# Kernel optimization log

Measured on AMD Instinct MI355X. Metric: run time of the kernel, lower is better.

The kernel has to match this reference:

```python
import jax, jax.numpy as jnp
from jax import lax
import numpy as np

DN = ('NCDHW', 'OIDHW', 'NCDHW')
ACTIVE_THRESH = 1


def setup_inputs() -> dict:
    key = jax.random.key(0)
    ks = jax.random.split(key, 10)
    B, D = 4, 64
    chans = [3, 64, 128, 256, 512]
    inp = {
        'x': jax.random.normal(ks[0], (B, 3, D, D, D), jnp.float32),
        'mask': jax.random.randint(ks[1], (B, D, D, D), 0, 20, jnp.int32),
    }
    for i in range(4):
        cin, cout = chans[i], chans[i + 1]
        fan_in = cin * 27
        scale = 1.0 / np.sqrt(fan_in)
        inp[f'w{i+1}'] = jax.random.normal(ks[2 + 2 * i], (cout, cin, 3, 3, 3), jnp.float32) * scale
        inp[f'b{i+1}'] = jax.random.normal(ks[3 + 2 * i], (cout,), jnp.float32) * scale
    return inp


def _sparse_block(x, m, w, b, stride):
    # SparseConv3d(k=3, pad=1) + SparseReLU: output active where 3^3 footprint hits an active input;
    # bias + relu applied only at active sites, inactive sites stay exactly 0 (spconv .dense() semantics).
    s = (stride,) * 3
    pad = [(1, 1)] * 3
    y = lax.conv_general_dilated(x, w, s, pad, dimension_numbers=DN)
    ones = jnp.ones((1, 1, 3, 3, 3), x.dtype)
    m_out = lax.conv_general_dilated(m[:, None].astype(x.dtype), ones, s, pad, dimension_numbers=DN) > 0
    y = jnp.where(m_out, jax.nn.relu(y + b[None, :, None, None, None]), jnp.zeros((), x.dtype))
    return y, m_out[:, 0]


def reference(x, mask, w1, b1, w2, b2, w3, b3, w4, b4):
    m = mask < ACTIVE_THRESH                       # [B,D,H,W] active voxels
    h = x * m[:, None].astype(x.dtype)             # zero inactive input features
    h, m = _sparse_block(h, m, w1, b1, 1)          # [B,64,64,64,64]
    h, m = _sparse_block(h, m, w2, b2, 2)          # [B,128,32,32,32]
    h, m = _sparse_block(h, m, w3, b3, 2)          # [B,256,16,16,16]
    h, m = _sparse_block(h, m, w4, b4, 2)          # [B,512,8,8,8]
    pooled = jnp.max(h, axis=(2, 3, 4))            # dense() + amax over D,H,W -> [B,512]
    return jax.nn.leaky_relu(pooled, negative_slope=0.2)
```

## Files before the change

### kernel.cpp

```cpp
#include <hip/hip_runtime.h>

typedef _Float16 f16;
typedef _Float16 half4 __attribute__((ext_vector_type(4)));
typedef _Float16 half8 __attribute__((ext_vector_type(8)));
typedef float f32x4 __attribute__((ext_vector_type(4)));

#define BATCH 4

__device__ __forceinline__ void gload16(const void* g, void* l) {
  __builtin_amdgcn_global_load_lds((const __attribute__((address_space(1))) unsigned int*)g,
                                   (__attribute__((address_space(3))) unsigned int*)l, 16, 0, 0);
}

__global__ __launch_bounds__(256) void zero_k(unsigned int* __restrict__ z) {
  z[threadIdx.x] = 0u;
}

__global__ __launch_bounds__(256) void wprep_k(const float* __restrict__ w,
                                               f16* __restrict__ w27, int COUT, int CIN) {
  int idx = blockIdx.x * 256 + threadIdx.x;
  int total = COUT * CIN * 27;
  if (idx >= total) return;
  int k = idx % 27;
  int t = idx / 27;
  int ci = t % CIN;
  int co = t / CIN;
  w27[((size_t)k * COUT + co) * CIN + ci] = (f16)w[idx];
}

__global__ __launch_bounds__(256) void wprep1_k(const float* __restrict__ w,
                                                f16* __restrict__ wf) {
  int idx = blockIdx.x * 256 + threadIdx.x;
  if (idx >= 64 * 128) return;
  int q = idx & 127, co = idx >> 7;
  int k = q >> 2, ci = q & 3;
  float v = (ci < 3 && k < 27) ? w[(co * 3 + ci) * 27 + k] : 0.f;
  wf[idx] = (f16)v;
}

__global__ __launch_bounds__(256) void xmask_k(const float* __restrict__ x,
                                               const int* __restrict__ mask,
                                               f16* __restrict__ xc) {
  const int D3 = 262144;
  int v = blockIdx.x * 256 + threadIdx.x;
  int b = blockIdx.y;
  bool act = mask[(size_t)b * D3 + v] < 1;
  const float* xb = x + (size_t)b * 3 * D3 + v;
  half4 o;
  o[0] = act ? (f16)xb[0] : (f16)0.f;
  o[1] = act ? (f16)xb[D3] : (f16)0.f;
  o[2] = act ? (f16)xb[2 * D3] : (f16)0.f;
  o[3] = (f16)0.f;
  *reinterpret_cast<half4*>(xc + ((size_t)b * D3 + v) * 4) = o;
}

__global__ __launch_bounds__(256) void dil_w_k(const int* __restrict__ mask,
                                               unsigned char* __restrict__ aw) {
  const int D3 = 262144;
  int t = blockIdx.x * 256 + threadIdx.x;
  int b = t >> 16;
  int v = (t & 65535) * 4;
  int w0 = v & 63;
  const int* mb = mask + (size_t)b * D3;
  int a[6];
  a[0] = (w0 > 0) ? (mb[v - 1] < 1) : 0;
  #pragma unroll
  for (int i = 0; i < 4; i++) a[i + 1] = mb[v + i] < 1;
  a[5] = (w0 < 60) ? (mb[v + 4] < 1) : 0;
  unsigned int o = 0;
  #pragma unroll
  for (int i = 0; i < 4; i++)
    o |= ((unsigned)(a[i] | a[i + 1] | a[i + 2])) << (8 * i);
  *reinterpret_cast<unsigned int*>(aw + (size_t)b * D3 + v) = o;
}

template<int STRIDE, int DIMSHIFT>
__global__ __launch_bounds__(256) void dil_hd_k(const unsigned char* __restrict__ ai,
                                                unsigned char* __restrict__ ao) {
  const int D3 = 262144;
  int t = blockIdx.x * 256 + threadIdx.x;
  int b = t >> 16;
  int v = (t & 65535) * 4;
  int c = (v >> DIMSHIFT) & 63;
  const unsigned char* ib = ai + (size_t)b * D3;
  unsigned int m = *reinterpret_cast<const unsigned int*>(ib + v);
  if (c > 0)  m |= *reinterpret_cast<const unsigned int*>(ib + v - STRIDE);
  if (c < 63) m |= *reinterpret_cast<const unsigned int*>(ib + v + STRIDE);
  *reinterpret_cast<unsigned int*>(ao + (size_t)b * D3 + v) = m;
}

template<int DIN, int DOUT>
__global__ __launch_bounds__(256) void dilate_s2_k(const unsigned char* __restrict__ mi,
                                                   unsigned char* __restrict__ mo) {
  const int Do3 = DOUT * DOUT * DOUT;
  int v = blockIdx.x * 256 + threadIdx.x;
  if (v >= Do3) return;
  int b = blockIdx.y;
  int ow = v % DOUT, t = v / DOUT, oh = t % DOUT, od = t / DOUT;
  const unsigned char* ib = mi + (size_t)b * DIN * DIN * DIN;
  int act = 0;
  for (int kd = 0; kd < 3; kd++) { int id = od * 2 - 1 + kd; if ((unsigned)id >= (unsigned)DIN) continue;
    for (int kh = 0; kh < 3; kh++) { int ih = oh * 2 - 1 + kh; if ((unsigned)ih >= (unsigned)DIN) continue;
      for (int kw = 0; kw < 3; kw++) { int iw = ow * 2 - 1 + kw; if ((unsigned)iw >= (unsigned)DIN) continue;
        act |= ib[((size_t)id * DIN + ih) * DIN + iw];
      } } }
  mo[(size_t)b * Do3 + v] = (unsigned char)(act ? 1 : 0);
}

template<int BM>
__global__ __launch_bounds__(256) void conv1_mfma_k(const f16* __restrict__ xc,
                                                    const f16* __restrict__ w1f,
                                                    const float* __restrict__ bias,
                                                    const unsigned char* __restrict__ mo,
                                                    f16* __restrict__ out) {
  const int D = 64, D3 = D * D * D, COUT = 64;
  constexpr int K = 128, LD = K + 8;
  constexpr int WM = 2, WN = 2;
  constexpr int MF = BM / (16 * WM), NF = 64 / (16 * WN);
  __shared__ __align__(16) f16 As[BM][LD];
  __shared__ __align__(16) f16 Bs[64][LD];

  const int tid = threadIdx.x, lane = tid & 63, wave = tid >> 6;
  const int wm = wave >> 1, wn = wave & 1;
  const int v0 = blockIdx.x * BM;
  const int b = blockIdx.y;
  const f16* xb = xc + (size_t)b * D3 * 4;

  for (int c = tid; c < 64 * (K / 8); c += 256) {
    int row = c >> 4, cc = c & 15;
    *reinterpret_cast<half8*>(&Bs[row][cc * 8]) =
        *reinterpret_cast<const half8*>(w1f + row * K + cc * 8);
  }
  {
    const int row = tid & (BM - 1);
    const int v = v0 + row;
    const int ow = v & 63, oh = (v >> 6) & 63, od = v >> 12;
    for (int e = tid; e < 32 * BM; e += 256) {
      int kslot = e / BM;
      half4 val = {};
      if (kslot < 27) {
        int kd = kslot / 9, r2 = kslot - kd * 9, kh = r2 / 3, kw = r2 - kh * 3;
        int id = od - 1 + kd, ih = oh - 1 + kh, iw = ow - 1 + kw;
        if ((unsigned)id < (unsigned)D && (unsigned)ih < (unsigned)D && (unsigned)iw < (unsigned)D)
          val = *reinterpret_cast<const half4*>(xb + (size_t)((id * D + ih) * D + iw) * 4);
      }
      *reinterpret_cast<half4*>(&As[row][kslot * 4]) = val;
    }
  }
  __syncthreads();

  f32x4 acc[MF][NF] = {};
  const int chanoff = (lane >> 4) << 3;
  const int arow = wm * MF * 16 + (lane & 15);
  const int brow = wn * NF * 16 + (lane & 15);
  #pragma unroll
  for (int q0 = 0; q0 < K; q0 += 32) {
    half8 a[MF], bb[NF];
    #pragma unroll
    for (int mf = 0; mf < MF; mf++)
      a[mf] = *reinterpret_cast<const half8*>(&As[arow + mf * 16][q0 + chanoff]);
    #pragma unroll
    for (int nf = 0; nf < NF; nf++)
      bb[nf] = *reinterpret_cast<const half8*>(&Bs[brow + nf * 16][q0 + chanoff]);
    #pragma unroll
    for (int mf = 0; mf < MF; mf++)
      #pragma unroll
      for (int nf = 0; nf < NF; nf++)
        acc[mf][nf] = __builtin_amdgcn_mfma_f32_16x16x32_f16(a[mf], bb[nf], acc[mf][nf], 0, 0, 0);
  }

  const unsigned char* mb = mo + (size_t)b * D3;
  f16* ob = out + (size_t)b * D3 * COUT;
  float bv[NF];
  #pragma unroll
  for (int nf = 0; nf < NF; nf++) bv[nf] = bias[wn * NF * 16 + nf * 16 + (lane & 15)];
  #pragma unroll
  for (int mf = 0; mf < MF; mf++) {
    #pragma unroll
    for (int r = 0; r < 4; r++) {
      int v = v0 + wm * MF * 16 + mf * 16 + ((lane >> 4) << 2) + r;
      bool act = mb[v] != 0;
      #pragma unroll
      for (int nf = 0; nf < NF; nf++) {
        int co = wn * NF * 16 + nf * 16 + (lane & 15);
        float val = acc[mf][nf][r] + bv[nf];
        val = act ? (val > 0.f ? val : 0.f) : 0.f;
        ob[(size_t)v * COUT + co] = (f16)val;
      }
    }
  }
}

template<int CIN, int COUT, int DIN, int DOUT, int BM, int BN, int WM, int WN, int SWZ>
__global__ __launch_bounds__(WM * WN * 64) void conv_mfma2_k(const f16* __restrict__ in,
                                                             const f16* __restrict__ w27,
                                                             const float* __restrict__ bias,
                                                             const unsigned char* __restrict__ mo,
                                                             const f16* __restrict__ zpage,
                                                             f16* __restrict__ out) {
  constexpr int NW = WM * WN;
  constexpr int MF = BM / (16 * WM), NF = BN / (16 * WN);
  constexpr int ROWB = CIN * 2;
  constexpr int CHUNKS = ROWB / 16;
  constexpr int RPI = 64 / CHUNKS;
  constexpr int A_IW = BM / RPI / NW;
  constexpr int B_IW = BN / RPI / NW;
  constexpr int D3o = DOUT * DOUT * DOUT;
  constexpr int LOGD = (DOUT == 32) ? 5 : ((DOUT == 16) ? 4 : 3);

  __shared__ __align__(16) char As[2][BM * ROWB];
  __shared__ __align__(16) char Bs[2][BN * ROWB];

  const int tid = threadIdx.x, lane = tid & 63, wave = tid >> 6;
  const int wm = wave / WN, wn = wave % WN;
  int bx = blockIdx.x;
  if (SWZ) {
    int cpx = gridDim.x >> 3;
    bx = (bx & 7) * cpx + (bx >> 3);
  }
  const int v0 = bx * BM, co0 = blockIdx.y * BN, b = blockIdx.z;
  const char* ib = (const char*)(in + (size_t)b * DIN * DIN * DIN * CIN);

  const int lrow = lane / CHUNKS;
  const int lchunk = lane % CHUNKS;
  int a_od[A_IW], a_oh[A_IW], a_ow[A_IW], a_cb[A_IW];
  #pragma unroll
  for (int i = 0; i < A_IW; i++) {
    int r = (wave * A_IW + i) * RPI + lrow;
    int v = v0 + r;
    a_ow[i] = v & (DOUT - 1);
    a_oh[i] = (v >> LOGD) & (DOUT - 1);
    a_od[i] = v >> (2 * LOGD);
    a_cb[i] = (lchunk ^ (r & 7)) * 16;
  }
  size_t b_ob[B_IW];
  #pragma unroll
  for (int i = 0; i < B_IW; i++) {
    int r = (wave * B_IW + i) * RPI + lrow;
    int g = lchunk ^ (r & 7);
    b_ob[i] = ((size_t)(co0 + r) * CIN + g * 8) * 2;
  }

  auto stage = [&](int buf, int k) {
    int kd = k / 9, r2 = k - kd * 9, kh = r2 / 3, kw = r2 - kh * 3;
    #pragma unroll
    for (int i = 0; i < A_IW; i++) {
      int id = 2 * a_od[i] - 1 + kd, ih = 2 * a_oh[i] - 1 + kh, iw = 2 * a_ow[i] - 1 + kw;
      bool inb = (unsigned)id < (unsigned)DIN && (unsigned)ih < (unsigned)DIN &&
                 (unsigned)iw < (unsigned)DIN;
      const char* src = inb
          ? ib + ((size_t)(id * DIN + ih) * DIN + iw) * ROWB + a_cb[i]
          : (const char*)zpage;
      gload16(src, &As[buf][(wave * A_IW + i) * 1024]);
    }
    const char* wk = (const char*)w27 + (size_t)k * COUT * CIN * 2;
    #pragma unroll
    for (int i = 0; i < B_IW; i++)
      gload16(wk + b_ob[i], &Bs[buf][(wave * B_IW + i) * 1024]);
  };

  f32x4 acc[MF][NF] = {};
  const int ll = lane & 15, lh = lane >> 4;
  const int ra0 = wm * MF * 16 + ll;
  const int rb0 = wn * NF * 16 + ll;
  const int rswa = ra0 & 7;
  const int rswb = rb0 & 7;

  stage(0, 0);
  __syncthreads();
  int cur = 0;
  for (int k = 0; k < 27; k++) {
    if (k < 26) stage(cur ^ 1, k + 1);
    #pragma unroll
    for (int ci0 = 0; ci0 < CIN; ci0 += 32) {
      const int q = (ci0 >> 3) + lh;
      half8 a[MF], bb[NF];
      #pragma unroll
      for (int mf = 0; mf < MF; mf++)
        a[mf] = *reinterpret_cast<const half8*>(
            &As[cur][(ra0 + mf * 16) * ROWB + ((q ^ rswa) * 16)]);
      #pragma unroll
      for (int nf = 0; nf < NF; nf++)
        bb[nf] = *reinterpret_cast<const half8*>(
            &Bs[cur][(rb0 + nf * 16) * ROWB + ((q ^ rswb) * 16)]);
      #pragma unroll
      for (int mf = 0; mf < MF; mf++)
        #pragma unroll
        for (int nf = 0; nf < NF; nf++)
          acc[mf][nf] = __builtin_amdgcn_mfma_f32_16x16x32_f16(a[mf], bb[nf], acc[mf][nf], 0, 0, 0);
    }
    __syncthreads();
    cur ^= 1;
  }

  const unsigned char* mb = mo + (size_t)b * D3o;
  f16* ob = out + (size_t)b * D3o * COUT;
  float bv[NF];
  #pragma unroll
  for (int nf = 0; nf < NF; nf++) bv[nf] = bias[co0 + wn * NF * 16 + nf * 16 + ll];
  #pragma unroll
  for (int mf = 0; mf < MF; mf++) {
    #pragma unroll
    for (int r = 0; r < 4; r++) {
      int v = v0 + wm * MF * 16 + mf * 16 + (lh << 2) + r;
      bool act = mb[v] != 0;
      #pragma unroll
      for (int nf = 0; nf < NF; nf++) {
        int co = co0 + wn * NF * 16 + nf * 16 + ll;
        float val = acc[mf][nf][r] + bv[nf];
        val = act ? (val > 0.f ? val : 0.f) : 0.f;
        ob[(size_t)v * COUT + co] = (f16)val;
      }
    }
  }
}

__global__ __launch_bounds__(256) void pool_k(const f16* __restrict__ h4,
                                              float* __restrict__ outp) {
  __shared__ float red[4][64];
  int b = blockIdx.y;
  int cl = threadIdx.x & 63;
  int co = blockIdx.x * 64 + cl;
  int vg = threadIdx.x >> 6;
  const f16* p = h4 + (size_t)b * 512 * 512;
  float m = 0.f;
  for (int v = vg * 128; v < vg * 128 + 128; v++) m = fmaxf(m, (float)p[(size_t)v * 512 + co]);
  red[vg][cl] = m;
  __syncthreads();
  if (threadIdx.x < 64) {
    m = fmaxf(fmaxf(red[0][threadIdx.x], red[1][threadIdx.x]),
              fmaxf(red[2][threadIdx.x], red[3][threadIdx.x]));
    float r = (m >= 0.f) ? m : 0.2f * m;
    outp[b * 512 + blockIdx.x * 64 + threadIdx.x] = r;
  }
}

extern "C" void kernel_launch(void* const* d_in, const int* in_sizes, int n_in,
                              void* d_out, int out_size, void* d_ws, size_t ws_size,
                              hipStream_t stream) {
  const float* x    = (const float*)d_in[0];
  const int*   mask = (const int*)d_in[1];
  const float* w1 = (const float*)d_in[2];
  const float* b1 = (const float*)d_in[3];
  const float* w2 = (const float*)d_in[4];
  const float* b2 = (const float*)d_in[5];
  const float* w3 = (const float*)d_in[6];
  const float* b3 = (const float*)d_in[7];
  const float* w4 = (const float*)d_in[8];
  const float* b4 = (const float*)d_in[9];
  float* outp = (float*)d_out;

  char* ws = (char*)d_ws;
  size_t off = 0;
  auto alloc = [&](size_t bytes) -> char* {
    char* p = ws + off;
    off = (off + bytes + 255) & ~(size_t)255;
    return p;
  };
  f16* wf1 = (f16*)alloc((size_t)64 * 128 * 2);
  f16* wf2 = (f16*)alloc((size_t)27 * 128 * 64 * 2);
  f16* wf3 = (f16*)alloc((size_t)27 * 256 * 128 * 2);
  f16* wf4 = (f16*)alloc((size_t)27 * 512 * 256 * 2);
  f16* zpg = (f16*)alloc(1024);
  f16* xc  = (f16*)alloc((size_t)BATCH * 262144 * 4 * 2);
  unsigned char* aw = (unsigned char*)alloc((size_t)BATCH * 262144);
  unsigned char* ah = (unsigned char*)alloc((size_t)BATCH * 262144);
  unsigned char* m1 = (unsigned char*)alloc((size_t)BATCH * 262144);
  unsigned char* m2 = (unsigned char*)alloc((size_t)BATCH * 32768);
  unsigned char* m3 = (unsigned char*)alloc((size_t)BATCH * 4096);
  unsigned char* m4 = (unsigned char*)alloc((size_t)BATCH * 512);
  f16* h1 = (f16*)alloc((size_t)BATCH * 262144 * 64 * 2);
  f16* h2 = (f16*)alloc((size_t)BATCH * 32768 * 128 * 2);
  f16* h3 = (f16*)alloc((size_t)BATCH * 4096 * 256 * 2);
  f16* h4 = (f16*)alloc((size_t)BATCH * 512 * 512 * 2);
  if (off > ws_size) return;

  zero_k<<<dim3(1), 256, 0, stream>>>((unsigned int*)zpg);
  wprep1_k<<<dim3((64 * 128 + 255) / 256), 256, 0, stream>>>(w1, wf1);
  wprep_k<<<dim3((128 * 64 * 27 + 255) / 256), 256, 0, stream>>>(w2, wf2, 128, 64);
  wprep_k<<<dim3((256 * 128 * 27 + 255) / 256), 256, 0, stream>>>(w3, wf3, 256, 128);
  wprep_k<<<dim3((512 * 256 * 27 + 255) / 256), 256, 0, stream>>>(w4, wf4, 512, 256);
  xmask_k<<<dim3(1024, BATCH), 256, 0, stream>>>(x, mask, xc);

  dil_w_k<<<dim3(BATCH * 65536 / 256), 256, 0, stream>>>(mask, aw);
  dil_hd_k<64, 6><<<dim3(BATCH * 65536 / 256), 256, 0, stream>>>(aw, ah);
  dil_hd_k<4096, 12><<<dim3(BATCH * 65536 / 256), 256, 0, stream>>>(ah, m1);
  dilate_s2_k<64, 32><<<dim3(128, BATCH), 256, 0, stream>>>(m1, m2);
  dilate_s2_k<32, 16><<<dim3(16, BATCH), 256, 0, stream>>>(m2, m3);
  dilate_s2_k<16, 8><<<dim3(2, BATCH), 256, 0, stream>>>(m3, m4);

  conv1_mfma_k<128><<<dim3(262144 / 128, BATCH), 256, 0, stream>>>(xc, wf1, b1, m1, h1);
  conv_mfma2_k<64, 128, 64, 32, 128, 128, 2, 2, 1>
      <<<dim3(256, 1, BATCH), 256, 0, stream>>>(h1, wf2, b2, m2, zpg, h2);
  conv_mfma2_k<128, 256, 32, 16, 64, 64, 2, 2, 0>
      <<<dim3(64, 4, BATCH), 256, 0, stream>>>(h2, wf3, b3, m3, zpg, h3);
  conv_mfma2_k<256, 512, 16, 8, 64, 64, 2, 2, 0>
      <<<dim3(8, 8, BATCH), 256, 0, stream>>>(h3, wf4, b4, m4, zpg, h4);

  pool_k<<<dim3(8, BATCH), 256, 0, stream>>>(h4, outp);
}
```

Baseline: 351.9 us.

## Store activations in zero-padded volumes to remove gather bounds checks

Activations and the masked input are written into volumes padded by one voxel on every side. Small new kernels zero the border voxels. The conv gather loops now add a constant per-tap offset to precomputed source pointers, so the per-load bounds checks, the zero-page fallback and the coordinate math are gone. In exchange the buffers grow slightly, several extra border-zeroing launches are added, and the padded input buffer reuses the layer-3 activation buffer's storage.

```diff
diff --git a/kernel.cpp b/kernel.cpp
--- a/kernel.cpp
+++ b/kernel.cpp
@@ -12,8 +12,18 @@
                                    (__attribute__((address_space(3))) unsigned int*)l, 16, 0, 0);
 }
 
-__global__ __launch_bounds__(256) void zero_k(unsigned int* __restrict__ z) {
-  z[threadIdx.x] = 0u;
+template<int DP, int ROWB>
+__global__ __launch_bounds__(256) void zborder_k(char* __restrict__ buf) {
+  int v = blockIdx.x * 256 + threadIdx.x;
+  int b = blockIdx.y;
+  if (v >= DP * DP * DP) return;
+  int w = v % DP; int t = v / DP; int h = t % DP; int d = t / DP;
+  bool border = (w == 0) | (w == DP - 1) | (h == 0) | (h == DP - 1) | (d == 0) | (d == DP - 1);
+  if (!border) return;
+  char* p = buf + ((size_t)b * DP * DP * DP + v) * ROWB;
+  #pragma unroll
+  for (int i = 0; i < ROWB; i += 8)
+    *reinterpret_cast<unsigned long long*>(p + i) = 0ull;
 }
 
 __global__ __launch_bounds__(256) void wprep_k(const float* __restrict__ w,
@@ -40,8 +50,8 @@
 
 __global__ __launch_bounds__(256) void xmask_k(const float* __restrict__ x,
                                                const int* __restrict__ mask,
-                                               f16* __restrict__ xc) {
-  const int D3 = 262144;
+                                               f16* __restrict__ xcp) {
+  const int D3 = 262144, PD = 66, PD3 = PD * PD * PD;
   int v = blockIdx.x * 256 + threadIdx.x;
   int b = blockIdx.y;
   bool act = mask[(size_t)b * D3 + v] < 1;
@@ -51,7 +61,9 @@
   o[1] = act ? (f16)xb[D3] : (f16)0.f;
   o[2] = act ? (f16)xb[2 * D3] : (f16)0.f;
   o[3] = (f16)0.f;
-  *reinterpret_cast<half4*>(xc + ((size_t)b * D3 + v) * 4) = o;
+  int ow = v & 63, oh = (v >> 6) & 63, od = v >> 12;
+  size_t pv = ((size_t)(od + 1) * PD + oh + 1) * PD + ow + 1;
+  *reinterpret_cast<half4*>(xcp + ((size_t)b * PD3 + pv) * 4) = o;
 }
 
 __global__ __launch_bounds__(256) void dil_w_k(const int* __restrict__ mask,
@@ -108,12 +120,12 @@
 }
 
 template<int BM>
-__global__ __launch_bounds__(256) void conv1_mfma_k(const f16* __restrict__ xc,
+__global__ __launch_bounds__(256) void conv1_mfma_k(const f16* __restrict__ xcp,
                                                     const f16* __restrict__ w1f,
                                                     const float* __restrict__ bias,
                                                     const unsigned char* __restrict__ mo,
-                                                    f16* __restrict__ out) {
-  const int D = 64, D3 = D * D * D, COUT = 64;
+                                                    f16* __restrict__ out ) {
+  const int D3 = 262144, COUT = 64, PD = 66, PD3 = PD * PD * PD;
   constexpr int K = 128, LD = K + 8;
   constexpr int WM = 2, WN = 2;
   constexpr int MF = BM / (16 * WM), NF = 64 / (16 * WN);
@@ -124,7 +136,7 @@
   const int wm = wave >> 1, wn = wave & 1;
   const int v0 = blockIdx.x * BM;
   const int b = blockIdx.y;
-  const f16* xb = xc + (size_t)b * D3 * 4;
+  const f16* xb = xcp + (size_t)b * PD3 * 4;
 
   for (int c = tid; c < 64 * (K / 8); c += 256) {
     int row = c >> 4, cc = c & 15;
@@ -135,14 +147,13 @@
     const int row = tid & (BM - 1);
     const int v = v0 + row;
     const int ow = v & 63, oh = (v >> 6) & 63, od = v >> 12;
+    const int base = (od * PD + oh) * PD + ow;
     for (int e = tid; e < 32 * BM; e += 256) {
       int kslot = e / BM;
       half4 val = {};
       if (kslot < 27) {
         int kd = kslot / 9, r2 = kslot - kd * 9, kh = r2 / 3, kw = r2 - kh * 3;
-        int id = od - 1 + kd, ih = oh - 1 + kh, iw = ow - 1 + kw;
-        if ((unsigned)id < (unsigned)D && (unsigned)ih < (unsigned)D && (unsigned)iw < (unsigned)D)
-          val = *reinterpret_cast<const half4*>(xb + (size_t)((id * D + ih) * D + iw) * 4);
+        val = *reinterpret_cast<const half4*>(xb + (size_t)(base + (kd * PD + kh) * PD + kw) * 4);
       }
       *reinterpret_cast<half4*>(&As[row][kslot * 4]) = val;
     }
@@ -170,34 +181,37 @@
   }
 
   const unsigned char* mb = mo + (size_t)b * D3;
-  f16* ob = out + (size_t)b * D3 * COUT;
+  f16* ob = out + (size_t)b * PD3 * COUT;
+  const int ll = lane & 15, lh = lane >> 4;
   float bv[NF];
   #pragma unroll
-  for (int nf = 0; nf < NF; nf++) bv[nf] = bias[wn * NF * 16 + nf * 16 + (lane & 15)];
+  for (int nf = 0; nf < NF; nf++) bv[nf] = bias[wn * NF * 16 + nf * 16 + ll];
   #pragma unroll
   for (int mf = 0; mf < MF; mf++) {
     #pragma unroll
     for (int r = 0; r < 4; r++) {
-      int v = v0 + wm * MF * 16 + mf * 16 + ((lane >> 4) << 2) + r;
+      int v = v0 + wm * MF * 16 + mf * 16 + (lh << 2) + r;
       bool act = mb[v] != 0;
+      int ow = v & 63, oh = (v >> 6) & 63, od = v >> 12;
+      size_t pv = ((size_t)(od + 1) * PD + oh + 1) * PD + ow + 1;
       #pragma unroll
       for (int nf = 0; nf < NF; nf++) {
-        int co = wn * NF * 16 + nf * 16 + (lane & 15);
+        int co = wn * NF * 16 + nf * 16 + ll;
         float val = acc[mf][nf][r] + bv[nf];
         val = act ? (val > 0.f ? val : 0.f) : 0.f;
-        ob[(size_t)v * COUT + co] = (f16)val;
+        ob[pv * COUT + co] = (f16)val;
       }
     }
   }
 }
 
-template<int CIN, int COUT, int DIN, int DOUT, int BM, int BN, int WM, int WN, int SWZ>
+template<int CIN, int COUT, int DIN, int DOUT, int BM, int BN, int WM, int WN, int SWZ, int OP>
 __global__ __launch_bounds__(WM * WN * 64) void conv_mfma2_k(const f16* __restrict__ in,
                                                              const f16* __restrict__ w27,
                                                              const float* __restrict__ bias,
                                                              const unsigned char* __restrict__ mo,
-                                                             const f16* __restrict__ zpage,
                                                              f16* __restrict__ out) {
+  constexpr int PD = DIN + 2, PDo = DOUT + 2;
   constexpr int NW = WM * WN;
   constexpr int MF = BM / (16 * WM), NF = BN / (16 * WN);
   constexpr int ROWB = CIN * 2;
@@ -219,44 +233,37 @@
     bx = (bx & 7) * cpx + (bx >> 3);
   }
   const int v0 = bx * BM, co0 = blockIdx.y * BN, b = blockIdx.z;
-  const char* ib = (const char*)(in + (size_t)b * DIN * DIN * DIN * CIN);
+  const char* ib = (const char*)(in + (size_t)b * PD * PD * PD * CIN);
 
   const int lrow = lane / CHUNKS;
   const int lchunk = lane % CHUNKS;
-  int a_od[A_IW], a_oh[A_IW], a_ow[A_IW], a_cb[A_IW];
+  const char* a_src[A_IW];
   #pragma unroll
   for (int i = 0; i < A_IW; i++) {
     int r = (wave * A_IW + i) * RPI + lrow;
     int v = v0 + r;
-    a_ow[i] = v & (DOUT - 1);
-    a_oh[i] = (v >> LOGD) & (DOUT - 1);
-    a_od[i] = v >> (2 * LOGD);
-    a_cb[i] = (lchunk ^ (r & 7)) * 16;
-  }
-  size_t b_ob[B_IW];
+    int ow = v & (DOUT - 1), oh = (v >> LOGD) & (DOUT - 1), od = v >> (2 * LOGD);
+    size_t flat = ((size_t)(2 * od) * PD + 2 * oh) * PD + 2 * ow;
+    a_src[i] = ib + flat * ROWB + (lchunk ^ (r & 7)) * 16;
+  }
+  const char* b_src[B_IW];
   #pragma unroll
   for (int i = 0; i < B_IW; i++) {
     int r = (wave * B_IW + i) * RPI + lrow;
     int g = lchunk ^ (r & 7);
-    b_ob[i] = ((size_t)(co0 + r) * CIN + g * 8) * 2;
+    b_src[i] = (const char*)w27 + ((size_t)(co0 + r) * CIN + g * 8) * 2;
   }
 
   auto stage = [&](int buf, int k) {
     int kd = k / 9, r2 = k - kd * 9, kh = r2 / 3, kw = r2 - kh * 3;
-    #pragma unroll
-    for (int i = 0; i < A_IW; i++) {
-      int id = 2 * a_od[i] - 1 + kd, ih = 2 * a_oh[i] - 1 + kh, iw = 2 * a_ow[i] - 1 + kw;
-      bool inb = (unsigned)id < (unsigned)DIN && (unsigned)ih < (unsigned)DIN &&
-                 (unsigned)iw < (unsigned)DIN;
-      const char* src = inb
-          ? ib + ((size_t)(id * DIN + ih) * DIN + iw) * ROWB + a_cb[i]
-          : (const char*)zpage;
-      gload16(src, &As[buf][(wave * A_IW + i) * 1024]);
-    }
-    const char* wk = (const char*)w27 + (size_t)k * COUT * CIN * 2;
+    int koff = ((kd * PD + kh) * PD + kw) * ROWB;
+    #pragma unroll
+    for (int i = 0; i < A_IW; i++)
+      gload16(a_src[i] + koff, &As[buf][(wave * A_IW + i) * 1024]);
+    size_t wko = (size_t)k * COUT * CIN * 2;
     #pragma unroll
     for (int i = 0; i < B_IW; i++)
-      gload16(wk + b_ob[i], &Bs[buf][(wave * B_IW + i) * 1024]);
+      gload16(b_src[i] + wko, &Bs[buf][(wave * B_IW + i) * 1024]);
   };
 
   f32x4 acc[MF][NF] = {};
@@ -294,7 +301,7 @@
   }
 
   const unsigned char* mb = mo + (size_t)b * D3o;
-  f16* ob = out + (size_t)b * D3o * COUT;
+  f16* ob = out + (size_t)b * (OP ? PDo * PDo * PDo : D3o) * COUT;
   float bv[NF];
   #pragma unroll
   for (int nf = 0; nf < NF; nf++) bv[nf] = bias[co0 + wn * NF * 16 + nf * 16 + ll];
@@ -304,12 +311,14 @@
     for (int r = 0; r < 4; r++) {
       int v = v0 + wm * MF * 16 + mf * 16 + (lh << 2) + r;
       bool act = mb[v] != 0;
+      int ow = v & (DOUT - 1), oh = (v >> LOGD) & (DOUT - 1), od = v >> (2 * LOGD);
+      size_t pv = OP ? (((size_t)(od + 1) * PDo + oh + 1) * PDo + ow + 1) : (size_t)v;
       #pragma unroll
       for (int nf = 0; nf < NF; nf++) {
         int co = co0 + wn * NF * 16 + nf * 16 + ll;
         float val = acc[mf][nf][r] + bv[nf];
         val = act ? (val > 0.f ? val : 0.f) : 0.f;
-        ob[(size_t)v * COUT + co] = (f16)val;
+        ob[pv * COUT + co] = (f16)val;
       }
     }
   }
@@ -350,6 +359,10 @@
   const float* b4 = (const float*)d_in[9];
   float* outp = (float*)d_out;
 
+  const size_t PD1 = 66 * 66 * 66;
+  const size_t PD2 = 34 * 34 * 34;
+  const size_t PD3s = 18 * 18 * 18;
+
   char* ws = (char*)d_ws;
   size_t off = 0;
   auto alloc = [&](size_t bytes) -> char* {
@@ -361,26 +374,23 @@
   f16* wf2 = (f16*)alloc((size_t)27 * 128 * 64 * 2);
   f16* wf3 = (f16*)alloc((size_t)27 * 256 * 128 * 2);
   f16* wf4 = (f16*)alloc((size_t)27 * 512 * 256 * 2);
-  f16* zpg = (f16*)alloc(1024);
-  f16* xc  = (f16*)alloc((size_t)BATCH * 262144 * 4 * 2);
   unsigned char* aw = (unsigned char*)alloc((size_t)BATCH * 262144);
   unsigned char* ah = (unsigned char*)alloc((size_t)BATCH * 262144);
   unsigned char* m1 = (unsigned char*)alloc((size_t)BATCH * 262144);
   unsigned char* m2 = (unsigned char*)alloc((size_t)BATCH * 32768);
   unsigned char* m3 = (unsigned char*)alloc((size_t)BATCH * 4096);
   unsigned char* m4 = (unsigned char*)alloc((size_t)BATCH * 512);
-  f16* h1 = (f16*)alloc((size_t)BATCH * 262144 * 64 * 2);
-  f16* h2 = (f16*)alloc((size_t)BATCH * 32768 * 128 * 2);
-  f16* h3 = (f16*)alloc((size_t)BATCH * 4096 * 256 * 2);
-  f16* h4 = (f16*)alloc((size_t)BATCH * 512 * 512 * 2);
+  f16* h1p = (f16*)alloc((size_t)BATCH * PD1 * 64 * 2);
+  f16* h2p = (f16*)alloc((size_t)BATCH * PD2 * 128 * 2);
+  f16* h3p = (f16*)alloc((size_t)BATCH * PD3s * 256 * 2);
+  f16* h4  = (f16*)alloc((size_t)BATCH * 512 * 512 * 2);
+  f16* xcp = h3p;
   if (off > ws_size) return;
 
-  zero_k<<<dim3(1), 256, 0, stream>>>((unsigned int*)zpg);
   wprep1_k<<<dim3((64 * 128 + 255) / 256), 256, 0, stream>>>(w1, wf1);
   wprep_k<<<dim3((128 * 64 * 27 + 255) / 256), 256, 0, stream>>>(w2, wf2, 128, 64);
   wprep_k<<<dim3((256 * 128 * 27 + 255) / 256), 256, 0, stream>>>(w3, wf3, 256, 128);
   wprep_k<<<dim3((512 * 256 * 27 + 255) / 256), 256, 0, stream>>>(w4, wf4, 512, 256);
-  xmask_k<<<dim3(1024, BATCH), 256, 0, stream>>>(x, mask, xc);
 
   dil_w_k<<<dim3(BATCH * 65536 / 256), 256, 0, stream>>>(mask, aw);
   dil_hd_k<64, 6><<<dim3(BATCH * 65536 / 256), 256, 0, stream>>>(aw, ah);
@@ -389,13 +399,21 @@
   dilate_s2_k<32, 16><<<dim3(16, BATCH), 256, 0, stream>>>(m2, m3);
   dilate_s2_k<16, 8><<<dim3(2, BATCH), 256, 0, stream>>>(m3, m4);
 
-  conv1_mfma_k<128><<<dim3(262144 / 128, BATCH), 256, 0, stream>>>(xc, wf1, b1, m1, h1);
-  conv_mfma2_k<64, 128, 64, 32, 128, 128, 2, 2, 1>
-      <<<dim3(256, 1, BATCH), 256, 0, stream>>>(h1, wf2, b2, m2, zpg, h2);
-  conv_mfma2_k<128, 256, 32, 16, 64, 64, 2, 2, 0>
-      <<<dim3(64, 4, BATCH), 256, 0, stream>>>(h2, wf3, b3, m3, zpg, h3);
-  conv_mfma2_k<256, 512, 16, 8, 64, 64, 2, 2, 0>
-      <<<dim3(8, 8, BATCH), 256, 0, stream>>>(h3, wf4, b4, m4, zpg, h4);
+  xmask_k<<<dim3(1024, BATCH), 256, 0, stream>>>(x, mask, xcp);
+  zborder_k<66, 8><<<dim3((287496 + 255) / 256, BATCH), 256, 0, stream>>>((char*)xcp);
+  zborder_k<66, 128><<<dim3((287496 + 255) / 256, BATCH), 256, 0, stream>>>((char*)h1p);
+  zborder_k<34, 256><<<dim3((39304 + 255) / 256, BATCH), 256, 0, stream>>>((char*)h2p);
+
+  conv1_mfma_k<128><<<dim3(262144 / 128, BATCH), 256, 0, stream>>>(xcp, wf1, b1, m1, h1p);
+
+  zborder_k<18, 512><<<dim3((5832 + 255) / 256, BATCH), 256, 0, stream>>>((char*)h3p);
+
+  conv_mfma2_k<64, 128, 64, 32, 128, 128, 2, 2, 1, 1>
+      <<<dim3(256, 1, BATCH), 256, 0, stream>>>(h1p, wf2, b2, m2, h2p);
+  conv_mfma2_k<128, 256, 32, 16, 64, 64, 2, 2, 0, 1>
+      <<<dim3(64, 4, BATCH), 256, 0, stream>>>(h2p, wf3, b3, m3, h3p);
+  conv_mfma2_k<256, 512, 16, 8, 64, 64, 2, 2, 0, 0>
+      <<<dim3(8, 8, BATCH), 256, 0, stream>>>(h3p, wf4, b4, m4, h4);
 
   pool_k<<<dim3(8, BATCH), 256, 0, stream>>>(h4, outp);
 }
```

Result: slower. 369.9 us (+5.1%).
